# Kernel tuning notes

Measured on AMD Instinct MI355X. Metric: run time of the kernel, lower is better.

## Reference

```python
import jax, jax.numpy as jnp
import numpy as np
import math

B, S, HID = 2, 2048, 1024
NH, HD = 16, 64
MAX_SEQ = 65536  # RoPE base from RotaryEmbedding


def _rope_tables(seq_len, dim):
    inv_freq = 1.0 / (MAX_SEQ ** (jnp.arange(0, dim, 2, dtype=jnp.float32) / dim))
    t = jnp.arange(seq_len, dtype=jnp.float32)
    freqs = jnp.einsum('i,j->ij', t, inv_freq)          # [S, dim/2]
    emb = jnp.concatenate([freqs, freqs], axis=-1)      # [S, dim]
    return jnp.cos(emb), jnp.sin(emb)


def _rotate_half(x):
    x1, x2 = jnp.split(x, 2, axis=-1)
    return jnp.concatenate([-x2, x1], axis=-1)


def setup_inputs() -> dict:
    key = jax.random.key(0)
    ks = jax.random.split(key, 9)
    std_qkv = 1.0 / math.sqrt(NH * HD)
    std_o = 1.0 / math.sqrt(HID)
    return {
        'input_embeds': jax.random.normal(ks[0], (B, S, HID), dtype=jnp.float32),
        'Wq': jax.random.normal(ks[1], (NH * HD, HID), dtype=jnp.float32) * std_qkv,
        'bq': jnp.zeros((NH * HD,), dtype=jnp.float32),
        'Wk': jax.random.normal(ks[2], (NH * HD, HID), dtype=jnp.float32) * std_qkv,
        'bk': jnp.zeros((NH * HD,), dtype=jnp.float32),
        'Wv': jax.random.normal(ks[3], (NH * HD, HID), dtype=jnp.float32) * std_qkv,
        'bv': jnp.zeros((NH * HD,), dtype=jnp.float32),
        'Wo': jax.random.normal(ks[4], (HID, NH * HD), dtype=jnp.float32) * std_o,
        'bo': jnp.zeros((HID,), dtype=jnp.float32),
    }


def reference(input_embeds, Wq, bq, Wk, bk, Wv, bv, Wo, bo):
    x = input_embeds
    b, s, _ = x.shape
    # QKV projections (torch Linear: x @ W.T + b)
    q = x @ Wq.T + bq
    k = x @ Wk.T + bk
    v = x @ Wv.T + bv
    # [B, S, NH*HD] -> [B, NH, S, HD]
    q = q.reshape(b, s, NH, HD).transpose(0, 2, 1, 3)
    k = k.reshape(b, s, NH, HD).transpose(0, 2, 1, 3)
    v = v.reshape(b, s, NH, HD).transpose(0, 2, 1, 3)
    # RoPE
    cos, sin = _rope_tables(s, HD)  # [S, HD]
    q = q * cos + _rotate_half(q) * sin
    k = k * cos + _rotate_half(k) * sin
    # SDPA (non-causal, no mask)
    scale = 1.0 / math.sqrt(HD)
    scores = jnp.einsum('bhqd,bhkd->bhqk', q, k) * scale
    attn = jax.nn.softmax(scores, axis=-1)
    out = jnp.einsum('bhqk,bhkd->bhqd', attn, v)
    # [B, NH, S, HD] -> [B, S, NH*HD]
    out = out.transpose(0, 2, 1, 3).reshape(b, s, NH * HD)
    return out @ Wo.T + bo
```

## Files before the change

kernel.cpp:

```cpp
#include <hip/hip_runtime.h>
#include <cstdint>
#include <cstddef>

#define S_LEN 2048
#define NHEAD 16
#define HDIM  64
#define HID_  1024

typedef short s8v  __attribute__((ext_vector_type(8)));
typedef short s4v  __attribute__((ext_vector_type(4)));
typedef float f4v  __attribute__((ext_vector_type(4)));
typedef float f16v __attribute__((ext_vector_type(16)));

__device__ __forceinline__ short f2b(float x) {
    union { float f; unsigned u; } a; a.f = x;
    unsigned r = a.u + 0x7fffu + ((a.u >> 16) & 1u);
    return (short)(r >> 16);
}

__device__ __forceinline__ void gload_lds16(const void* g, void* l) {
    __builtin_amdgcn_global_load_lds(
        (__attribute__((address_space(1))) void*)const_cast<void*>(g),
        (__attribute__((address_space(3))) void*)l, 16, 0, 0);
}

__device__ __forceinline__ unsigned cvtpk(float a, float b) {
    unsigned r;
    asm("v_cvt_pk_bf16_f32 %0, %1, %2" : "=v"(r) : "v"(a), "v"(b));
    return r;
}
__device__ __forceinline__ void plswap(unsigned& a, unsigned& b) {
    asm("v_permlane32_swap_b32 %0, %1" : "+v"(a), "+v"(b));
}

__global__ __launch_bounds__(256) void f2b_kernel(const float* __restrict__ in,
                                                  short* __restrict__ out, int n4) {
    int i = blockIdx.x * 256 + threadIdx.x;
    if (i >= n4) return;
    float4 v = reinterpret_cast<const float4*>(in)[i];
    s4v o;
    o[0] = f2b(v.x); o[1] = f2b(v.y); o[2] = f2b(v.z); o[3] = f2b(v.w);
    reinterpret_cast<s4v*>(out)[i] = o;
}

__global__ __launch_bounds__(256) void f2bw_kernel(
    const float* __restrict__ Wq, const float* __restrict__ Wk,
    const float* __restrict__ Wv, const float* __restrict__ Wo,
    short* __restrict__ Wcat, short* __restrict__ Wob)
{
    const int y = blockIdx.y;
    const float* src = (y == 0) ? Wq : (y == 1) ? Wk : (y == 2) ? Wv : Wo;
    short* dst = (y < 3) ? (Wcat + (size_t)y * 1048576) : Wob;
    int i = blockIdx.x * 256 + threadIdx.x;
    float4 v = reinterpret_cast<const float4*>(src)[i];
    s4v o;
    o[0] = f2b(v.x); o[1] = f2b(v.y); o[2] = f2b(v.z); o[3] = f2b(v.w);
    reinterpret_cast<s4v*>(dst)[i] = o;
}

__global__ __launch_bounds__(256) void rope_table_kernel(float2* __restrict__ tab) {
    int idx = blockIdx.x * 256 + threadIdx.x;
    int s = idx >> 5, j = idx & 31;
    float inv = exp2f(-0.5f * (float)j);
    float ang = (float)s * inv;
    float2 cs; cs.x = cosf(ang); cs.y = sinf(ang);
    tab[idx] = cs;
}

__global__ __launch_bounds__(256) void gemm_qkv(
    const short* __restrict__ A, const short* __restrict__ Bw,
    const float* __restrict__ bq, const float* __restrict__ bk,
    const float* __restrict__ bv,
    short* __restrict__ Qo, short* __restrict__ Ko, short* __restrict__ Vo,
    const float2* __restrict__ rtab)
{
    __shared__ short Asl[2][128 * 32];
    __shared__ short Bsl[2][128 * 32];
    const int t = threadIdx.x;
    const int lane = t & 63;
    const int l15 = lane & 15, l4 = lane >> 4;
    const int wid = t >> 6;
    const int blk = blockIdx.x;
    const int x = blk & 7, j = blk >> 3;
    const int tn = (x * 3 + j % 3) * 128;
    const int tm = (j / 3) * 128;
    const int K = 1024;
    const int wrow = (wid >> 1) * 64, wcol = (wid & 1) * 64;

    f4v acc[4][4];
#pragma unroll
    for (int i = 0; i < 4; ++i)
#pragma unroll
        for (int jj = 0; jj < 4; ++jj) acc[i][jj] = (f4v){0.f, 0.f, 0.f, 0.f};

    const int r0 = t >> 2;
    const int c0 = (t & 3) * 8;
    const int wbase = (t & ~63) * 8;

#define QSTAGE(buf, kt) do { const int k0_ = (kt) << 5;                            \
        gload_lds16(A  + (size_t)(tm + r0)      * K + k0_ + c0, &Asl[buf][wbase]);        \
        gload_lds16(A  + (size_t)(tm + 64 + r0) * K + k0_ + c0, &Asl[buf][2048 + wbase]); \
        gload_lds16(Bw + (size_t)(tn + r0)      * K + k0_ + c0, &Bsl[buf][wbase]);        \
        gload_lds16(Bw + (size_t)(tn + 64 + r0) * K + k0_ + c0, &Bsl[buf][2048 + wbase]); \
    } while (0)

    QSTAGE(0, 0);
    __syncthreads();
    int cur = 0;
    for (int kt = 0; kt < 32; ++kt) {
        if (kt < 31) QSTAGE(cur ^ 1, kt + 1);
        s8v af[4], bf[4];
#pragma unroll
        for (int i = 0; i < 4; ++i) {
            af[i] = *(const s8v*)&Asl[cur][(wrow + i * 16 + l15) * 32 + 8 * l4];
            bf[i] = *(const s8v*)&Bsl[cur][(wcol + i * 16 + l15) * 32 + 8 * l4];
        }
#pragma unroll
        for (int i = 0; i < 4; ++i)
#pragma unroll
            for (int jj = 0; jj < 4; ++jj)
                acc[i][jj] = __builtin_amdgcn_mfma_f32_16x16x32_bf16(af[i], bf[jj], acc[i][jj], 0, 0, 0);
        __syncthreads();
        cur ^= 1;
    }
#undef QSTAGE

    const int mode = tn >> 10;
    const float* bias = (mode == 0) ? bq : (mode == 1) ? bk : bv;
    short* outb = (mode == 0) ? Qo : (mode == 1) ? Ko : Vo;

    if (mode == 2) {
#pragma unroll
        for (int i = 0; i < 4; ++i) {
            int rowb = tm + wrow + i * 16 + l4 * 4;
            int b_ = rowb >> 11, s0 = rowb & 2047;
#pragma unroll
            for (int jj = 0; jj < 4; ++jj) {
                int col = tn + wcol + jj * 16 + l15;
                int cm = col & 1023;
                float bvv = bias[cm];
                int h = cm >> 6, d = col & 63;
                s4v o4;
#pragma unroll
                for (int r = 0; r < 4; ++r) o4[r] = f2b(acc[i][jj][r] + bvv);
                *(s4v*)&outb[((size_t)((b_ * NHEAD + h) * 64 + d)) * S_LEN + s0] = o4;
            }
        }
    } else {
        int h = ((tn & 1023) + wcol) >> 6;
        const float osc = (mode == 0) ? 0.180336880111f : 1.0f;
#pragma unroll
        for (int i = 0; i < 4; ++i) {
#pragma unroll
            for (int r = 0; r < 4; ++r) {
                int row = tm + wrow + i * 16 + l4 * 4 + r;
                int b_ = row >> 11, s = row & 2047;
                float2 cs0 = rtab[(s << 5) + l15];
                float2 cs1 = rtab[(s << 5) + 16 + l15];
#pragma unroll
                for (int jj = 0; jj < 4; ++jj) {
                    int col = tn + wcol + jj * 16 + l15;
                    int cm = col & 1023;
                    int d = col & 63;
                    float v  = acc[i][jj][r]     + bias[cm];
                    float vp = acc[i][jj ^ 2][r] + bias[cm ^ 32];
                    float2 cs = (jj & 1) ? cs1 : cs0;
                    float res = (d < 32) ? (v * cs.x - vp * cs.y)
                                         : (v * cs.x + vp * cs.y);
                    outb[(((size_t)(b_ * NHEAD + h) * S_LEN + s) << 6) + d] = f2b(res * osc);
                }
            }
        }
    }
}

__global__ __launch_bounds__(256) void gemm_o(
    const short* __restrict__ A, const short* __restrict__ Bw,
    const float* __restrict__ bias, float* __restrict__ outf)
{
    __shared__ short Asl[2][64 * 32];
    __shared__ short Bsl[2][128 * 32];
    const int t = threadIdx.x;
    const int lane = t & 63;
    const int l15 = lane & 15, l4 = lane >> 4;
    const int wid = t >> 6;
    const int blk = blockIdx.x;
    const int tn = (blk & 7) * 128;
    const int tm = (blk >> 3) * 64;
    const int K = 1024, N = 1024;
    const int wrow = (wid >> 1) * 32, wcol = (wid & 1) * 64;

    f4v acc[2][4];
#pragma unroll
    for (int i = 0; i < 2; ++i)
#pragma unroll
        for (int jj = 0; jj < 4; ++jj) acc[i][jj] = (f4v){0.f, 0.f, 0.f, 0.f};

    const int r0 = t >> 2;
    const int c0 = (t & 3) * 8;
    const int wbase = (t & ~63) * 8;

#define OSTAGE(buf, kt) do { const int k0_ = (kt) << 5;                            \
        gload_lds16(A  + (size_t)(tm + r0)      * K + k0_ + c0, &Asl[buf][wbase]);        \
        gload_lds16(Bw + (size_t)(tn + r0)      * K + k0_ + c0, &Bsl[buf][wbase]);        \
        gload_lds16(Bw + (size_t)(tn + 64 + r0) * K + k0_ + c0, &Bsl[buf][2048 + wbase]); \
    } while (0)

    OSTAGE(0, 0);
    __syncthreads();
    int cur = 0;
    for (int kt = 0; kt < 32; ++kt) {
        if (kt < 31) OSTAGE(cur ^ 1, kt + 1);
        s8v af[2], bf[4];
#pragma unroll
        for (int i = 0; i < 2; ++i)
            af[i] = *(const s8v*)&Asl[cur][(wrow + i * 16 + l15) * 32 + 8 * l4];
#pragma unroll
        for (int jj = 0; jj < 4; ++jj)
            bf[jj] = *(const s8v*)&Bsl[cur][(wcol + jj * 16 + l15) * 32 + 8 * l4];
#pragma unroll
        for (int i = 0; i < 2; ++i)
#pragma unroll
            for (int jj = 0; jj < 4; ++jj)
                acc[i][jj] = __builtin_amdgcn_mfma_f32_16x16x32_bf16(af[i], bf[jj], acc[i][jj], 0, 0, 0);
        __syncthreads();
        cur ^= 1;
    }
#undef OSTAGE

#pragma unroll
    for (int i = 0; i < 2; ++i) {
        int rowb = tm + wrow + i * 16 + l4 * 4;
#pragma unroll
        for (int jj = 0; jj < 4; ++jj) {
            int col = tn + wcol + jj * 16 + l15;
            float bv = bias[col];
#pragma unroll
            for (int r = 0; r < 4; ++r)
                outf[(size_t)(rowb + r) * N + col] = acc[i][jj][r] + bv;
        }
    }
}

#define SWB(row, bofs) ((bofs) ^ (((row) & 7) << 4))

__global__ __launch_bounds__(256) void attn2_kernel(
    const short* __restrict__ Q, const short* __restrict__ K,
    const short* __restrict__ Vt, short* __restrict__ O)
{
    __shared__ short Kl[2][4096];
    __shared__ short Vl[2][4096];

    const int t = threadIdx.x, lane = t & 63, wid = t >> 6;
    const int q5 = lane & 31, hi = lane >> 5;

    const int blk = blockIdx.x;
    const int x = blk & 7, j = blk >> 3;
    const int bh = x * 4 + (j & 3), qb = j >> 2;

    const short* Qb = Q + (size_t)bh * S_LEN * 64;
    const char*  Kb = (const char*)(K  + (size_t)bh * S_LEN * 64);
    const char*  Vb = (const char*)(Vt + (size_t)bh * S_LEN * 64);
    const int qrow = qb * 128 + wid * 32 + q5;

    s8v qf[4];
#pragma unroll
    for (int sl = 0; sl < 4; ++sl)
        qf[sl] = *(const s8v*)&Qb[(size_t)qrow * 64 + sl * 16 + hi * 8];

    f16v oacc[2];
#pragma unroll
    for (int dt = 0; dt < 2; ++dt)
#pragma unroll
        for (int e = 0; e < 16; ++e) oacc[dt][e] = 0.f;
    float m2 = -1e30f, lsum = 0.f;

    const int skey  = t >> 3;
    const int sboff = (t & 7) * 16;
    const int ssw   = SWB(skey, sboff);
    const size_t koffB = (size_t)skey * 128  + ssw;
    const size_t voffB = (size_t)skey * 4096 + ssw;

#define STAGE(buf, kb) do {                                                        \
        gload_lds16(Kb + (size_t)(kb) * 128 + koffB,              &Kl[buf][wid * 512]);        \
        gload_lds16(Kb + (size_t)(kb) * 128 + koffB + 32 * 128,   &Kl[buf][2048 + wid * 512]); \
        gload_lds16(Vb + (size_t)(kb) * 2   + voffB,              &Vl[buf][wid * 512]);        \
        gload_lds16(Vb + (size_t)(kb) * 2   + voffB + 32 * 4096,  &Vl[buf][2048 + wid * 512]); \
    } while (0)

    STAGE(0, 0);
    __syncthreads();

    int cur = 0;
    for (int kt = 0; kt < S_LEN / 64; ++kt) {
        if (kt < S_LEN / 64 - 1) STAGE(cur ^ 1, (kt + 1) * 64);

        f16v sc[2];
#pragma unroll
        for (int c = 0; c < 2; ++c) {
#pragma unroll
            for (int e = 0; e < 16; ++e) sc[c][e] = 0.f;
            const int krow = c * 32 + q5;
            const char* kbase = (const char*)&Kl[cur][0] + krow * 128;
            __builtin_amdgcn_s_setprio(1);
#pragma unroll
            for (int sl = 0; sl < 4; ++sl) {
                s8v kf = *(const s8v*)(kbase + SWB(krow, sl * 32 + hi * 16));
                sc[c] = __builtin_amdgcn_mfma_f32_32x32x16_bf16(kf, qf[sl], sc[c], 0, 0, 0);
            }
            __builtin_amdgcn_s_setprio(0);
        }

        float pm = -1e30f;
#pragma unroll
        for (int c = 0; c < 2; ++c)
#pragma unroll
            for (int e = 0; e < 16; e += 2)
                pm = fmaxf(pm, fmaxf(sc[c][e], sc[c][e + 1]));
        pm = fmaxf(pm, __shfl_xor(pm, 32, 64));
        if (__any(pm > m2 + 8.0f)) {
            float m2n = fmaxf(m2, pm);
            float fr = __builtin_amdgcn_exp2f(m2 - m2n);
            lsum *= fr;
#pragma unroll
            for (int dt = 0; dt < 2; ++dt)
#pragma unroll
                for (int e = 0; e < 16; ++e) oacc[dt][e] *= fr;
            m2 = m2n;
        }
        float ps = 0.f;
#pragma unroll
        for (int c = 0; c < 2; ++c)
#pragma unroll
            for (int e = 0; e < 16; ++e) {
                float p = __builtin_amdgcn_exp2f(sc[c][e] - m2);
                sc[c][e] = p;
                ps += p;
            }
        lsum += ps;

#pragma unroll
        for (int c = 0; c < 2; ++c) {
#pragma unroll
            for (int ks = 0; ks < 2; ++ks) {
                const int b0 = ks * 8;
                unsigned x0 = cvtpk(sc[c][b0 + 0], sc[c][b0 + 1]);
                unsigned y0 = cvtpk(sc[c][b0 + 4], sc[c][b0 + 5]);
                unsigned x1 = cvtpk(sc[c][b0 + 2], sc[c][b0 + 3]);
                unsigned y1 = cvtpk(sc[c][b0 + 6], sc[c][b0 + 7]);
                plswap(x0, y0);
                plswap(x1, y1);
                union { unsigned u[4]; s8v s; } pf;
                pf.u[0] = x0; pf.u[1] = x1; pf.u[2] = y0; pf.u[3] = y1;
                __builtin_amdgcn_s_setprio(1);
#pragma unroll
                for (int dt = 0; dt < 2; ++dt) {
                    const int vrow = dt * 32 + q5;
                    s8v vf = *(const s8v*)((const char*)&Vl[cur][0] + vrow * 128 +
                                           SWB(vrow, c * 64 + ks * 32 + hi * 16));
                    oacc[dt] = __builtin_amdgcn_mfma_f32_32x32x16_bf16(vf, pf.s, oacc[dt], 0, 0, 0);
                }
                __builtin_amdgcn_s_setprio(0);
            }
        }

        __syncthreads();
        cur ^= 1;
    }

    float ls = lsum + __shfl_xor(lsum, 32, 64);
    float inv = 1.0f / ls;
    const int b_ = bh >> 4, h = bh & 15;
    const size_t rbase = ((size_t)(b_ * S_LEN + qrow)) * HID_ + h * 64;
#pragma unroll
    for (int dt = 0; dt < 2; ++dt)
#pragma unroll
        for (int g = 0; g < 4; ++g) {
            s4v o4;
#pragma unroll
            for (int jj = 0; jj < 4; ++jj) o4[jj] = f2b(oacc[dt][g * 4 + jj] * inv);
            const int d0 = dt * 32 + g * 8 + hi * 4;
            *(s4v*)&O[rbase + d0] = o4;
        }
}

extern "C" void kernel_launch(void* const* d_in, const int* in_sizes, int n_in,
                              void* d_out, int out_size, void* d_ws, size_t ws_size,
                              hipStream_t stream)
{
    const float* X  = (const float*)d_in[0];
    const float* Wq = (const float*)d_in[1];
    const float* bq = (const float*)d_in[2];
    const float* Wk = (const float*)d_in[3];
    const float* bk = (const float*)d_in[4];
    const float* Wv = (const float*)d_in[5];
    const float* bv = (const float*)d_in[6];
    const float* Wo = (const float*)d_in[7];
    const float* bo = (const float*)d_in[8];
    float* out = (float*)d_out;

    char* ws = (char*)d_ws;
    short*  Xb   = (short*) (ws);
    short*  Wcat = (short*) (ws + ( 8u << 20));
    short*  Wob  = (short*) (ws + (14u << 20));
    float2* rtab = (float2*)(ws + (16u << 20));
    short*  Qbh  = (short*) (ws + (17u << 20));
    short*  Kbh  = (short*) (ws + (25u << 20));
    short*  Vbh  = (short*) (ws + (33u << 20));
    short*  Obf  = (short*) (ws + (41u << 20));

    f2b_kernel<<<4096, 256, 0, stream>>>(X, Xb, 1048576);
    f2bw_kernel<<<dim3(1024, 4), 256, 0, stream>>>(Wq, Wk, Wv, Wo, Wcat, Wob);
    rope_table_kernel<<<256, 256, 0, stream>>>(rtab);

    gemm_qkv<<<768, 256, 0, stream>>>(Xb, Wcat, bq, bk, bv, Qbh, Kbh, Vbh, rtab);
    attn2_kernel<<<512, 256, 0, stream>>>(Qbh, Kbh, Vbh, Obf);
    gemm_o<<<512, 256, 0, stream>>>(Obf, Wob, bo, out);
}
```

Baseline: 151.0 us.

## Split attention over two key halves and merge with a combine kernel

Splits each attention block's key range into two halves, doubling the grid to 1024 blocks. Each half writes a normalized bf16 partial output plus its row max and sum to scratch buffers, reusing the workspace and output memory. A new combine kernel reweights and merges the two partials into the head-interleaved layout. This aims to raise occupancy and CU utilization on the attention stage, at the cost of an extra launch, extra memory traffic, and an added bf16 rounding of the partials.

```diff
diff --git a/kernel.cpp b/kernel.cpp
--- a/kernel.cpp
+++ b/kernel.cpp
@@ -16,6 +16,10 @@
     union { float f; unsigned u; } a; a.f = x;
     unsigned r = a.u + 0x7fffu + ((a.u >> 16) & 1u);
     return (short)(r >> 16);
+}
+__device__ __forceinline__ float b2f(short x) {
+    union { unsigned u; float f; } a; a.u = ((unsigned)(unsigned short)x) << 16;
+    return a.f;
 }
 
 __device__ __forceinline__ void gload_lds16(const void* g, void* l) {
@@ -244,9 +248,10 @@
 
 #define SWB(row, bofs) ((bofs) ^ (((row) & 7) << 4))
 
-__global__ __launch_bounds__(256) void attn2_kernel(
+__global__ __launch_bounds__(256) void attn_split(
     const short* __restrict__ Q, const short* __restrict__ K,
-    const short* __restrict__ Vt, short* __restrict__ O)
+    const short* __restrict__ Vt,
+    short* __restrict__ P0, short* __restrict__ P1, float2* __restrict__ ML)
 {
     __shared__ short Kl[2][4096];
     __shared__ short Vl[2][4096];
@@ -256,7 +261,10 @@
 
     const int blk = blockIdx.x;
     const int x = blk & 7, j = blk >> 3;
-    const int bh = x * 4 + (j & 3), qb = j >> 2;
+    const int bh = x * 4 + (j & 3);
+    const int rest = j >> 2;
+    const int qb = rest & 15, split = rest >> 4;
+    const int kt0 = split * 16;
 
     const short* Qb = Q + (size_t)bh * S_LEN * 64;
     const char*  Kb = (const char*)(K  + (size_t)bh * S_LEN * 64);
@@ -288,12 +296,12 @@
         gload_lds16(Vb + (size_t)(kb) * 2   + voffB + 32 * 4096,  &Vl[buf][2048 + wid * 512]); \
     } while (0)
 
-    STAGE(0, 0);
+    STAGE(0, kt0 * 64);
     __syncthreads();
 
     int cur = 0;
-    for (int kt = 0; kt < S_LEN / 64; ++kt) {
-        if (kt < S_LEN / 64 - 1) STAGE(cur ^ 1, (kt + 1) * 64);
+    for (int kt = kt0; kt < kt0 + 16; ++kt) {
+        if (kt < kt0 + 15) STAGE(cur ^ 1, (kt + 1) * 64);
 
         f16v sc[2];
 #pragma unroll
@@ -370,8 +378,7 @@
 
     float ls = lsum + __shfl_xor(lsum, 32, 64);
     float inv = 1.0f / ls;
-    const int b_ = bh >> 4, h = bh & 15;
-    const size_t rbase = ((size_t)(b_ * S_LEN + qrow)) * HID_ + h * 64;
+    short* Pp = (split ? P1 : P0) + ((size_t)bh * S_LEN + qrow) * 64;
 #pragma unroll
     for (int dt = 0; dt < 2; ++dt)
 #pragma unroll
@@ -380,8 +387,36 @@
 #pragma unroll
             for (int jj = 0; jj < 4; ++jj) o4[jj] = f2b(oacc[dt][g * 4 + jj] * inv);
             const int d0 = dt * 32 + g * 8 + hi * 4;
-            *(s4v*)&O[rbase + d0] = o4;
-        }
+            *(s4v*)&Pp[d0] = o4;
+        }
+    if (hi == 0) {
+        float2 ml; ml.x = m2; ml.y = ls;
+        ML[(size_t)split * (32 * S_LEN) + bh * S_LEN + qrow] = ml;
+    }
+}
+
+__global__ __launch_bounds__(256) void attn_combine(
+    const short* __restrict__ P0, const short* __restrict__ P1,
+    const float2* __restrict__ ML, short* __restrict__ Obf)
+{
+    int idx = blockIdx.x * 256 + threadIdx.x;
+    int row = idx >> 3;
+    int d0 = (idx & 7) * 8;
+    float2 a = ML[row];
+    float2 b = ML[32 * S_LEN + row];
+    float m = fmaxf(a.x, b.x);
+    float w0 = a.y * exp2f(a.x - m);
+    float w1 = b.y * exp2f(b.x - m);
+    float inv = 1.0f / (w0 + w1);
+    w0 *= inv; w1 *= inv;
+    s8v v0 = *(const s8v*)&P0[(size_t)row * 64 + d0];
+    s8v v1 = *(const s8v*)&P1[(size_t)row * 64 + d0];
+    s8v o;
+#pragma unroll
+    for (int e = 0; e < 8; ++e) o[e] = f2b(w0 * b2f(v0[e]) + w1 * b2f(v1[e]));
+    int bh = row >> 11, s = row & 2047;
+    int b_ = bh >> 4, h = bh & 15;
+    *(s8v*)&Obf[((size_t)(b_ * S_LEN + s)) * HID_ + h * 64 + d0] = o;
 }
 
 extern "C" void kernel_launch(void* const* d_in, const int* in_sizes, int n_in,
@@ -408,12 +443,16 @@
     short*  Kbh  = (short*) (ws + (25u << 20));
     short*  Vbh  = (short*) (ws + (33u << 20));
     short*  Obf  = (short*) (ws + (41u << 20));
+    short*  P0   = (short*) (ws);
+    short*  P1   = (short*) d_out;
+    float2* ML   = (float2*)((char*)d_out + (8u << 20));
 
     f2b_kernel<<<4096, 256, 0, stream>>>(X, Xb, 1048576);
     f2bw_kernel<<<dim3(1024, 4), 256, 0, stream>>>(Wq, Wk, Wv, Wo, Wcat, Wob);
     rope_table_kernel<<<256, 256, 0, stream>>>(rtab);
 
     gemm_qkv<<<768, 256, 0, stream>>>(Xb, Wcat, bq, bk, bv, Qbh, Kbh, Vbh, rtab);
-    attn2_kernel<<<512, 256, 0, stream>>>(Qbh, Kbh, Vbh, Obf);
+    attn_split<<<1024, 256, 0, stream>>>(Qbh, Kbh, Vbh, P0, P1, ML);
+    attn_combine<<<2048, 256, 0, stream>>>(P0, P1, ML, Obf);
     gemm_o<<<512, 256, 0, stream>>>(Obf, Wob, bo, out);
 }
```

New measurement: 157.8 us. +4.5%, slower.
